# Performance work log

Measured on AMD Instinct MI355X. Metric: run time of the kernel, lower is better.

Reference implementation:

```python
import math
import jax, jax.numpy as jnp
import numpy as np

B, S, H, DQ, DV = 2, 2048, 16, 192, 128
NEG_INF = jnp.float32(-1e30)


def setup_inputs() -> dict:
    key = jax.random.key(0)
    kq, kk, kv = jax.random.split(key, 3)
    q = jax.random.normal(kq, (B, S, H, DQ), dtype=jnp.float32)
    k = jax.random.normal(kk, (B, S, H, DQ), dtype=jnp.float32)
    v = jax.random.normal(kv, (B, S, H, DV), dtype=jnp.float32)
    return {"q": q, "k": k, "v": v}


def reference(q, k, v):
    # Causal MLA attention, BSHD layout, asymmetric QK vs V head dims.
    dq = q.shape[-1]
    scale = jnp.asarray(math.sqrt(1.0 / dq), dtype=q.dtype)  # default 1/sqrt(dq)
    # scores: [B, H, S, S]
    scores = jnp.einsum("bqhd,bkhd->bhqk", q, k) * scale
    s = q.shape[1]
    causal = jnp.tril(jnp.ones((s, s), dtype=bool))  # qidx >= kidx
    scores = jnp.where(causal[None, None, :, :], scores, NEG_INF)
    p = jax.nn.softmax(scores, axis=-1)
    # out: [B, S, H, DV]
    out = jnp.einsum("bhqk,bkhd->bqhd", p, v)
    return out
```

## Files before the change

### kernel.cpp

```cpp
#include <hip/hip_runtime.h>

#define B_ 2
#define S_ 2048
#define H_ 16
#define DQ_ 192
#define DV_ 128
#define SCL2 0.10411163731422901f

typedef short short8 __attribute__((ext_vector_type(8)));
typedef float f32x4 __attribute__((ext_vector_type(4)));
typedef unsigned uint2v __attribute__((ext_vector_type(2)));

#define KG_BYTES ((size_t)25165824)
#define VG_BYTES ((size_t)16777216)

__device__ __forceinline__ unsigned short f2bf(float f) {
  union { float f; unsigned u; } x; x.f = f;
  unsigned r = x.u + 0x7FFFu + ((x.u >> 16) & 1u);
  return (unsigned short)(r >> 16);
}

__device__ __forceinline__ float hw_exp2(float x) {
  float r; asm("v_exp_f32 %0, %1" : "=v"(r) : "v"(x)); return r;
}
__device__ __forceinline__ unsigned cvtpk(float lo, float hi) {
  unsigned r; asm("v_cvt_pk_bf16_f32 %0, %1, %2" : "=v"(r) : "v"(lo), "v"(hi)); return r;
}
__device__ __forceinline__ float pl32max(float x) {
  uint2v r = __builtin_amdgcn_permlane32_swap(__float_as_uint(x), __float_as_uint(x), false, false);
  return fmaxf(__uint_as_float(r[0]), __uint_as_float(r[1]));
}
__device__ __forceinline__ float pl32add(float x) {
  uint2v r = __builtin_amdgcn_permlane32_swap(__float_as_uint(x), __float_as_uint(x), false, false);
  return __uint_as_float(r[0]) + __uint_as_float(r[1]);
}

#define GLL16(src, dst) \
  __builtin_amdgcn_global_load_lds((const __attribute__((address_space(1))) void*)(src), \
                                   (__attribute__((address_space(3))) void*)(dst), 16, 0, 0)

__global__ __launch_bounds__(256) void prep_k(const float* __restrict__ K,
                                              unsigned short* __restrict__ Kg) {
  int idx = blockIdx.x * 256 + threadIdx.x;
  int d4 = idx % 48; int r = idx / 48;
  int h = r % H_; r /= H_;
  int s = r % S_; int b = r / S_;
  float4 f = *(const float4*)(K + (size_t)((b * S_ + s) * H_ + h) * DQ_ + d4 * 4);
  ushort4 u; u.x = f2bf(f.x); u.y = f2bf(f.y); u.z = f2bf(f.z); u.w = f2bf(f.w);
  size_t rowb = (size_t)((b * H_ + h) * S_ + s) * (DQ_ * 2);
  int cb = (d4 * 8) ^ ((s & 7) << 4);
  *(ushort4*)((char*)Kg + rowb + cb) = u;
}

__global__ __launch_bounds__(256) void prep_v(const float* __restrict__ V,
                                              unsigned short* __restrict__ Vg) {
  __shared__ float lv[32][132];
  int blk = blockIdx.x;
  int sb = blk & 63, bh = blk >> 6;
  int b = bh >> 4, h = bh & 15;
  int tid = threadIdx.x;
  #pragma unroll
  for (int i = 0; i < 4; ++i) {
    int idx = i * 256 + tid;
    int s_in = idx >> 5, d4 = idx & 31;
    float4 f = *(const float4*)(V + (size_t)((b * S_ + sb * 32 + s_in) * H_ + h) * DV_ + d4 * 4);
    lv[s_in][d4 * 4 + 0] = f.x; lv[s_in][d4 * 4 + 1] = f.y;
    lv[s_in][d4 * 4 + 2] = f.z; lv[s_in][d4 * 4 + 3] = f.w;
  }
  __syncthreads();
  char* base = (char*)Vg + (size_t)blk * 8192;
  #pragma unroll
  for (int j = 0; j < 2; ++j) {
    int ob = tid * 32 + j * 16;
    int row = ob >> 7, cb = ob & 127;
    int orig = cb ^ ((row & 7) << 4);
    int d = row * 2 + (orig >> 6);
    int s0 = (orig & 63) >> 1;
    short8 u;
    #pragma unroll
    for (int e = 0; e < 8; ++e) u[e] = (short)f2bf(lv[s0 + e][d]);
    *(short8*)(base + ob) = u;
  }
}

__launch_bounds__(256, 2)
__global__ void mla_fwd(const float* __restrict__ Q,
                        const unsigned short* __restrict__ Kg,
                        const unsigned short* __restrict__ Vg,
                        float* __restrict__ O) {
  __shared__ __align__(16) unsigned char SB[2][20480];

  const int tid  = threadIdx.x;
  const int wid  = tid >> 6;
  const int lane = tid & 63;
  const int l15  = lane & 15;
  const int g    = lane >> 4;

  const int i  = blockIdx.x;
  const int x  = i & 7;
  const int li = i >> 3;
  const int j  = li & 15;
  const int bh = x * 4 + (li >> 4);
  const int b  = bh >> 4, h = bh & 15;

  const char* kg_bh = (const char*)Kg + (size_t)bh * S_ * (DQ_ * 2);
  const char* vg_bh = (const char*)Vg + (size_t)bh * 64 * 8192;

  const int kxor = (l15 & 7) << 4;
  const int g16  = g * 16;
  const int vlane = 12288 + (l15 >> 1) * 128 +
                    ((((l15 & 1) * 64) + g16) ^ (((l15 >> 1) & 7) << 4));
  const int sA = l15 + ((lane & 16) << 1);
  const int sB = sA + 16;
  const bool up = lane >= 32;

  #define STAGE(buf)                                         \
    do {                                                     \
      _Pragma("unroll")                                      \
      for (int ci = 0; ci < 5; ++ci) {                       \
        GLL16(sp[ci], &SB[buf][sdo[ci]]);                    \
        sp[ci] += sst[ci];                                   \
      }                                                      \
    } while (0)

  for (int job = 0; job < 2; ++job) {
    const int qtile = job ? j : (31 - j);
    const int q0w = qtile * 64 + wid * 16;

    short8 aq[6];
    {
      const size_t qoff = (size_t)((b * S_ + (q0w + l15)) * H_ + h) * DQ_;
      #pragma unroll
      for (int d0 = 0; d0 < 6; ++d0) {
        const float* p = Q + qoff + d0 * 32 + g * 8;
        float4 f0 = *(const float4*)(p);
        float4 f1 = *(const float4*)(p + 4);
        short8 a;
        a[0] = f2bf(f0.x * SCL2); a[1] = f2bf(f0.y * SCL2);
        a[2] = f2bf(f0.z * SCL2); a[3] = f2bf(f0.w * SCL2);
        a[4] = f2bf(f1.x * SCL2); a[5] = f2bf(f1.y * SCL2);
        a[6] = f2bf(f1.z * SCL2); a[7] = f2bf(f1.w * SCL2);
        aq[d0] = a;
      }
    }

    f32x4 o[8];
    #pragma unroll
    for (int t2 = 0; t2 < 8; ++t2) o[t2] = (f32x4)0.0f;
    float m = -1e30f, l = 0.0f;

    const int ntiles = qtile * 2 + 2;

    const char* sp[5];
    int sdo[5], sst[5];
    #pragma unroll
    for (int ci = 0; ci < 5; ++ci) {
      int cc = wid * 5 + ci;
      if (cc < 12) { sp[ci] = kg_bh + cc * 1024 + lane * 16;        sdo[ci] = cc * 1024;                sst[ci] = 12288; }
      else         { sp[ci] = vg_bh + (cc - 12) * 1024 + lane * 16; sdo[ci] = 12288 + (cc - 12) * 1024; sst[ci] = 8192; }
    }

    STAGE(0);
    __syncthreads();

    int cur = 0;
    for (int kt = 0; kt < ntiles; ++kt) {
      const int kbase = kt * 32;
      if (kt + 1 < ntiles) STAGE(cur ^ 1);

      const char* k0 = (const char*)&SB[cur][0] + l15 * 384;
      const char* k1 = k0 + 16 * 384;
      f32x4 sa0 = (f32x4)0.0f, sa1 = (f32x4)0.0f;
      __builtin_amdgcn_s_setprio(1);
      #pragma unroll
      for (int d0 = 0; d0 < 6; ++d0) {
        const int col = (d0 * 64 + g16) ^ kxor;
        short8 b0 = *(const short8*)(k0 + col);
        sa0 = __builtin_amdgcn_mfma_f32_16x16x32_bf16(b0, aq[d0], sa0, 0, 0, 0);
        short8 b1 = *(const short8*)(k1 + col);
        sa1 = __builtin_amdgcn_mfma_f32_16x16x32_bf16(b1, aq[d0], sa1, 0, 0, 0);
      }
      __builtin_amdgcn_s_setprio(0);

      const char* vbp = (const char*)&SB[cur][0] + vlane;
      short8 vb0 = *(const short8*)(vbp);
      short8 vb1 = *(const short8*)(vbp + 1024);
      short8 vb2 = *(const short8*)(vbp + 2048);
      short8 vb3 = *(const short8*)(vbp + 3072);

      float p[8];
      #pragma unroll
      for (int r = 0; r < 4; ++r) { p[r] = sa0[r]; p[4 + r] = sa1[r]; }
      if (kbase + 31 > q0w) {
        const int rem = q0w + l15 - kbase - 4 * g;
        #pragma unroll
        for (int r = 0; r < 4; ++r) {
          if (r > rem)      p[r]     = -1e30f;
          if (16 + r > rem) p[4 + r] = -1e30f;
        }
      }

      float mx = fmaxf(fmaxf(fmaxf(p[0], p[1]), fmaxf(p[2], p[3])),
                       fmaxf(fmaxf(p[4], p[5]), fmaxf(p[6], p[7])));
      mx = fmaxf(mx, __shfl_xor(mx, 16));
      mx = pl32max(mx);
      if (__any(mx > m + 8.0f)) {
        float mn = fmaxf(m, mx);
        float al = hw_exp2(m - mn);
        #pragma unroll
        for (int t2 = 0; t2 < 8; ++t2) o[t2] *= al;
        l *= al; m = mn;
      }
      #pragma unroll
      for (int jj = 0; jj < 8; ++jj) p[jj] = hw_exp2(p[jj] - m);
      l += ((p[0] + p[1]) + (p[2] + p[3])) + ((p[4] + p[5]) + (p[6] + p[7]));

      unsigned pk0 = cvtpk(p[0], p[1]);
      unsigned pk1 = cvtpk(p[2], p[3]);
      unsigned pk2 = cvtpk(p[4], p[5]);
      unsigned pk3 = cvtpk(p[6], p[7]);
      unsigned lo0 = __shfl(pk0, sA), hi0 = __shfl(pk2, sA);
      unsigned lo1 = __shfl(pk1, sA), hi1 = __shfl(pk3, sA);
      unsigned lo2 = __shfl(pk0, sB), hi2 = __shfl(pk2, sB);
      unsigned lo3 = __shfl(pk1, sB), hi3 = __shfl(pk3, sB);
      short8 vb4 = *(const short8*)(vbp + 4096);
      short8 vb5 = *(const short8*)(vbp + 5120);
      short8 vb6 = *(const short8*)(vbp + 6144);
      short8 vb7 = *(const short8*)(vbp + 7168);
      union { unsigned u[4]; short8 s; } pb;
      pb.u[0] = up ? hi0 : lo0;
      pb.u[1] = up ? hi1 : lo1;
      pb.u[2] = up ? hi2 : lo2;
      pb.u[3] = up ? hi3 : lo3;

      __builtin_amdgcn_s_setprio(1);
      o[0] = __builtin_amdgcn_mfma_f32_16x16x32_bf16(vb0, pb.s, o[0], 0, 0, 0);
      o[1] = __builtin_amdgcn_mfma_f32_16x16x32_bf16(vb1, pb.s, o[1], 0, 0, 0);
      o[2] = __builtin_amdgcn_mfma_f32_16x16x32_bf16(vb2, pb.s, o[2], 0, 0, 0);
      o[3] = __builtin_amdgcn_mfma_f32_16x16x32_bf16(vb3, pb.s, o[3], 0, 0, 0);
      o[4] = __builtin_amdgcn_mfma_f32_16x16x32_bf16(vb4, pb.s, o[4], 0, 0, 0);
      o[5] = __builtin_amdgcn_mfma_f32_16x16x32_bf16(vb5, pb.s, o[5], 0, 0, 0);
      o[6] = __builtin_amdgcn_mfma_f32_16x16x32_bf16(vb6, pb.s, o[6], 0, 0, 0);
      o[7] = __builtin_amdgcn_mfma_f32_16x16x32_bf16(vb7, pb.s, o[7], 0, 0, 0);
      __builtin_amdgcn_s_setprio(0);

      __syncthreads();
      cur ^= 1;
    }

    {
      float ll = l + __shfl_xor(l, 16);
      ll = pl32add(ll);
      const int q = q0w + l15;
      const float inv = 1.0f / ll;
      float* ob = O + (size_t)((b * S_ + q) * H_ + h) * DV_ + 4 * g;
      #pragma unroll
      for (int t2 = 0; t2 < 8; ++t2) {
        float4 st = { o[t2][0] * inv, o[t2][1] * inv, o[t2][2] * inv, o[t2][3] * inv };
        *(float4*)(ob + 16 * t2) = st;
      }
    }
  }
  #undef STAGE
}

__launch_bounds__(256)
__global__ void mla_fwd_fb(const float* __restrict__ Q,
                           const float* __restrict__ K,
                           const float* __restrict__ V,
                           float* __restrict__ O) {
  __shared__ __align__(16) unsigned short Kl[2][32][200];
  __shared__ __align__(16) unsigned short Vt[2][128][40];
  __shared__ __align__(16) unsigned short Pl[4][16][40];
  const int tid = threadIdx.x, wid = tid >> 6, lane = tid & 63;
  const int l15 = lane & 15, g = lane >> 4;
  const int qtile = (int)gridDim.x - 1 - (int)blockIdx.x;
  const int bh = blockIdx.y, b = bh >> 4, h = bh & 15;
  const int q0w = qtile * 64 + wid * 16;
  const int krs = H_ * DQ_, vrs = H_ * DV_;
  short8 aq[6];
  {
    const int qoff = ((b * S_ + (q0w + l15)) * H_ + h) * DQ_;
    #pragma unroll
    for (int d0 = 0; d0 < 6; ++d0) {
      const float* p = Q + qoff + d0 * 32 + g * 8;
      float4 f0 = *(const float4*)(p); float4 f1 = *(const float4*)(p + 4);
      short8 a;
      a[0]=f2bf(f0.x); a[1]=f2bf(f0.y); a[2]=f2bf(f0.z); a[3]=f2bf(f0.w);
      a[4]=f2bf(f1.x); a[5]=f2bf(f1.y); a[6]=f2bf(f1.z); a[7]=f2bf(f1.w);
      aq[d0] = a;
    }
  }
  f32x4 o[8];
  #pragma unroll
  for (int t = 0; t < 8; ++t) o[t] = (f32x4)0.0f;
  float m[4], l[4];
  #pragma unroll
  for (int r = 0; r < 4; ++r) { m[r] = -1e30f; l[r] = 0.0f; }
  const int ntiles = qtile * 2 + 2;
  float4 kr[6], vr[4];
  {
    const float* Kb = K + ((b * S_) * H_ + h) * DQ_;
    #pragma unroll
    for (int i = 0; i < 6; ++i) { int idx = i*256+tid; int row = idx/48, c4 = idx%48;
      kr[i] = *(const float4*)(Kb + row*krs + c4*4); }
    const float* Vb = V + ((b * S_) * H_ + h) * DV_;
    #pragma unroll
    for (int i = 0; i < 4; ++i) { int idx = i*256+tid; int row = idx&31, c4 = idx>>5;
      vr[i] = *(const float4*)(Vb + row*vrs + c4*4); }
    #pragma unroll
    for (int i = 0; i < 6; ++i) { int idx = i*256+tid; int row = idx/48, c4 = idx%48;
      ushort4 u; u.x=f2bf(kr[i].x); u.y=f2bf(kr[i].y); u.z=f2bf(kr[i].z); u.w=f2bf(kr[i].w);
      *(ushort4*)&Kl[0][row][c4*4] = u; }
    #pragma unroll
    for (int i = 0; i < 4; ++i) { int idx = i*256+tid; int row = idx&31, c4 = idx>>5;
      Vt[0][c4*4+0][row]=f2bf(vr[i].x); Vt[0][c4*4+1][row]=f2bf(vr[i].y);
      Vt[0][c4*4+2][row]=f2bf(vr[i].z); Vt[0][c4*4+3][row]=f2bf(vr[i].w); }
  }
  __syncthreads();
  int cur = 0;
  for (int kt = 0; kt < ntiles; ++kt) {
    const int kbase = kt * 32;
    const bool pf = (kt + 1 < ntiles);
    if (pf) {
      const int nb = kbase + 32;
      const float* Kb = K + ((b*S_+nb)*H_ + h)*DQ_;
      #pragma unroll
      for (int i = 0; i < 6; ++i) { int idx = i*256+tid; int row = idx/48, c4 = idx%48;
        kr[i] = *(const float4*)(Kb + row*krs + c4*4); }
      const float* Vb = V + ((b*S_+nb)*H_ + h)*DV_;
      #pragma unroll
      for (int i = 0; i < 4; ++i) { int idx = i*256+tid; int row = idx&31, c4 = idx>>5;
        vr[i] = *(const float4*)(Vb + row*vrs + c4*4); }
    }
    f32x4 sa0 = (f32x4)0.0f, sa1 = (f32x4)0.0f;
    #pragma unroll
    for (int d0 = 0; d0 < 6; ++d0) {
      short8 b0 = *(const short8*)&Kl[cur][l15][d0*32 + g*8];
      sa0 = __builtin_amdgcn_mfma_f32_16x16x32_bf16(aq[d0], b0, sa0, 0, 0, 0);
      short8 b1 = *(const short8*)&Kl[cur][16+l15][d0*32 + g*8];
      sa1 = __builtin_amdgcn_mfma_f32_16x16x32_bf16(aq[d0], b1, sa1, 0, 0, 0);
    }
    float p0[4], p1[4];
    #pragma unroll
    for (int r = 0; r < 4; ++r) {
      const int qg = q0w + 4*g + r;
      float s0 = sa0[r]*SCL2, s1 = sa1[r]*SCL2;
      if (kbase + l15 > qg) s0 = -1e30f;
      if (kbase + 16 + l15 > qg) s1 = -1e30f;
      p0[r] = s0; p1[r] = s1;
    }
    #pragma unroll
    for (int r = 0; r < 4; ++r) {
      float rm = fmaxf(p0[r], p1[r]);
      #pragma unroll
      for (int off = 1; off < 16; off <<= 1) rm = fmaxf(rm, __shfl_xor(rm, off));
      float mn = fmaxf(m[r], rm);
      float alpha = exp2f(m[r] - mn); m[r] = mn;
      float e0 = exp2f(p0[r] - mn), e1 = exp2f(p1[r] - mn);
      p0[r] = e0; p1[r] = e1;
      float rsum = e0 + e1;
      #pragma unroll
      for (int off = 1; off < 16; off <<= 1) rsum += __shfl_xor(rsum, off);
      l[r] = l[r]*alpha + rsum;
      #pragma unroll
      for (int t = 0; t < 8; ++t) o[t][r] *= alpha;
    }
    #pragma unroll
    for (int r = 0; r < 4; ++r) {
      Pl[wid][4*g+r][l15]      = f2bf(p0[r]);
      Pl[wid][4*g+r][16+l15]   = f2bf(p1[r]);
    }
    short8 pa = *(const short8*)&Pl[wid][l15][g*8];
    #pragma unroll
    for (int t = 0; t < 8; ++t) {
      short8 vb = *(const short8*)&Vt[cur][t*16+l15][g*8];
      o[t] = __builtin_amdgcn_mfma_f32_16x16x32_bf16(pa, vb, o[t], 0, 0, 0);
    }
    if (pf) {
      #pragma unroll
      for (int i = 0; i < 6; ++i) { int idx = i*256+tid; int row = idx/48, c4 = idx%48;
        ushort4 u; u.x=f2bf(kr[i].x); u.y=f2bf(kr[i].y); u.z=f2bf(kr[i].z); u.w=f2bf(kr[i].w);
        *(ushort4*)&Kl[cur^1][row][c4*4] = u; }
      #pragma unroll
      for (int i = 0; i < 4; ++i) { int idx = i*256+tid; int row = idx&31, c4 = idx>>5;
        Vt[cur^1][c4*4+0][row]=f2bf(vr[i].x); Vt[cur^1][c4*4+1][row]=f2bf(vr[i].y);
        Vt[cur^1][c4*4+2][row]=f2bf(vr[i].z); Vt[cur^1][c4*4+3][row]=f2bf(vr[i].w); }
    }
    __syncthreads();
    cur ^= 1;
  }
  #pragma unroll
  for (int r = 0; r < 4; ++r) {
    const int qg = q0w + 4*g + r;
    const float inv = 1.0f / l[r];
    #pragma unroll
    for (int t = 0; t < 8; ++t)
      O[((b*S_+qg)*H_ + h)*DV_ + t*16 + l15] = o[t][r] * inv;
  }
}

extern "C" void kernel_launch(void* const* d_in, const int* in_sizes, int n_in,
                              void* d_out, int out_size, void* d_ws, size_t ws_size,
                              hipStream_t stream) {
  const float* q = (const float*)d_in[0];
  const float* k = (const float*)d_in[1];
  const float* v = (const float*)d_in[2];
  float* out = (float*)d_out;

  if (ws_size >= KG_BYTES + VG_BYTES) {
    unsigned short* Kg = (unsigned short*)d_ws;
    unsigned short* Vg = (unsigned short*)((char*)d_ws + KG_BYTES);
    prep_k<<<dim3((B_ * S_ * H_ * 48) / 256), dim3(256), 0, stream>>>(k, Kg);
    prep_v<<<dim3(B_ * H_ * 64), dim3(256), 0, stream>>>(v, Vg);
    mla_fwd<<<dim3(512), dim3(256), 0, stream>>>(q, Kg, Vg, out);
  } else {
    dim3 grid(S_ / 64, B_ * H_);
    mla_fwd_fb<<<grid, dim3(256), 0, stream>>>(q, k, v, out);
  }
}
```

Before: 106.2 us.

## Switch attention to 32x32 MFMA with 128-row query tiles and 64-key stages

```diff
diff --git a/kernel.cpp b/kernel.cpp
--- a/kernel.cpp
+++ b/kernel.cpp
@@ -9,6 +9,7 @@
 
 typedef short short8 __attribute__((ext_vector_type(8)));
 typedef float f32x4 __attribute__((ext_vector_type(4)));
+typedef float f32x16 __attribute__((ext_vector_type(16)));
 typedef unsigned uint2v __attribute__((ext_vector_type(2)));
 
 #define KG_BYTES ((size_t)25165824)
@@ -54,32 +55,32 @@
 
 __global__ __launch_bounds__(256) void prep_v(const float* __restrict__ V,
                                               unsigned short* __restrict__ Vg) {
-  __shared__ float lv[32][132];
+  __shared__ float lv[64][132];
   int blk = blockIdx.x;
-  int sb = blk & 63, bh = blk >> 6;
+  int tile = blk & 31, bh = blk >> 5;
   int b = bh >> 4, h = bh & 15;
   int tid = threadIdx.x;
   #pragma unroll
-  for (int i = 0; i < 4; ++i) {
-    int idx = i * 256 + tid;
+  for (int it = 0; it < 8; ++it) {
+    int idx = it * 256 + tid;
     int s_in = idx >> 5, d4 = idx & 31;
-    float4 f = *(const float4*)(V + (size_t)((b * S_ + sb * 32 + s_in) * H_ + h) * DV_ + d4 * 4);
+    float4 f = *(const float4*)(V + (size_t)((b * S_ + tile * 64 + s_in) * H_ + h) * DV_ + d4 * 4);
     lv[s_in][d4 * 4 + 0] = f.x; lv[s_in][d4 * 4 + 1] = f.y;
     lv[s_in][d4 * 4 + 2] = f.z; lv[s_in][d4 * 4 + 3] = f.w;
   }
   __syncthreads();
-  char* base = (char*)Vg + (size_t)blk * 8192;
-  #pragma unroll
-  for (int j = 0; j < 2; ++j) {
-    int ob = tid * 32 + j * 16;
-    int row = ob >> 7, cb = ob & 127;
-    int orig = cb ^ ((row & 7) << 4);
-    int d = row * 2 + (orig >> 6);
-    int s0 = (orig & 63) >> 1;
+  char* base = (char*)Vg + (size_t)blk * 16384;
+  #pragma unroll
+  for (int it = 0; it < 4; ++it) {
+    int ch = it * 256 + tid;
+    int pr = ch >> 4, ci = ch & 15;
+    int orig = ci ^ (pr & 15);
+    int dv = pr * 2 + (orig >> 3);
+    int k0 = (orig & 7) * 8;
     short8 u;
     #pragma unroll
-    for (int e = 0; e < 8; ++e) u[e] = (short)f2bf(lv[s0 + e][d]);
-    *(short8*)(base + ob) = u;
+    for (int e = 0; e < 8; ++e) u[e] = (short)f2bf(lv[k0 + e][dv]);
+    *(short8*)(base + ch * 16) = u;
   }
 }
 
@@ -88,180 +89,177 @@
                         const unsigned short* __restrict__ Kg,
                         const unsigned short* __restrict__ Vg,
                         float* __restrict__ O) {
-  __shared__ __align__(16) unsigned char SB[2][20480];
+  __shared__ __align__(16) unsigned char SB[2][40960];
 
   const int tid  = threadIdx.x;
   const int wid  = tid >> 6;
   const int lane = tid & 63;
-  const int l15  = lane & 15;
-  const int g    = lane >> 4;
+  const int l31  = lane & 31;
+  const int hi   = lane >> 5;
+  const int hi16 = hi * 16;
 
   const int i  = blockIdx.x;
   const int x  = i & 7;
   const int li = i >> 3;
-  const int j  = li & 15;
-  const int bh = x * 4 + (li >> 4);
+  const int r_ = li >> 5;
+  const int c  = li & 31;
+  const int bh = x * 4 + (c >> 3);
+  const int jj = c & 7;
+  const int qtile = r_ ? jj : (15 - jj);
   const int b  = bh >> 4, h = bh & 15;
 
   const char* kg_bh = (const char*)Kg + (size_t)bh * S_ * (DQ_ * 2);
-  const char* vg_bh = (const char*)Vg + (size_t)bh * 64 * 8192;
-
-  const int kxor = (l15 & 7) << 4;
-  const int g16  = g * 16;
-  const int vlane = 12288 + (l15 >> 1) * 128 +
-                    ((((l15 & 1) * 64) + g16) ^ (((l15 >> 1) & 7) << 4));
-  const int sA = l15 + ((lane & 16) << 1);
-  const int sB = sA + 16;
-  const bool up = lane >= 32;
-
-  #define STAGE(buf)                                         \
-    do {                                                     \
-      _Pragma("unroll")                                      \
-      for (int ci = 0; ci < 5; ++ci) {                       \
-        GLL16(sp[ci], &SB[buf][sdo[ci]]);                    \
-        sp[ci] += sst[ci];                                   \
-      }                                                      \
+  const char* vg_bh = (const char*)Vg + (size_t)bh * 32 * 16384;
+
+  const int wq0 = qtile * 128 + wid * 32;
+  const int qln = wq0 + l31;
+
+  short8 qf[12];
+  {
+    const size_t qoff = (size_t)((b * S_ + qln) * H_ + h) * DQ_;
+    #pragma unroll
+    for (int d0 = 0; d0 < 12; ++d0) {
+      const float* p = Q + qoff + d0 * 16 + hi * 8;
+      float4 f0 = *(const float4*)(p);
+      float4 f1 = *(const float4*)(p + 4);
+      short8 a;
+      a[0] = f2bf(f0.x * SCL2); a[1] = f2bf(f0.y * SCL2);
+      a[2] = f2bf(f0.z * SCL2); a[3] = f2bf(f0.w * SCL2);
+      a[4] = f2bf(f1.x * SCL2); a[5] = f2bf(f1.y * SCL2);
+      a[6] = f2bf(f1.z * SCL2); a[7] = f2bf(f1.w * SCL2);
+      qf[d0] = a;
+    }
+  }
+
+  f32x16 o[4];
+  #pragma unroll
+  for (int t2 = 0; t2 < 4; ++t2) o[t2] = (f32x16)0.0f;
+  float m = -1e30f, l = 0.0f;
+
+  const int kxor = (lane & 7) << 4;
+  const int prl  = l31 >> 1;
+  const int nb_  = (lane & 1) * 8 + hi;
+  int voff[2][2];
+  #pragma unroll
+  for (int kh = 0; kh < 2; ++kh)
+    #pragma unroll
+    for (int ks = 0; ks < 2; ++ks) {
+      int n = nb_ + kh * 4 + ks * 2;
+      voff[kh][ks] = prl * 256 + ((n ^ prl) << 4);
+    }
+
+  const int ntiles = 2 * qtile + 2;
+
+  const char* kS = kg_bh + wid * 10240 + lane * 16;
+  const char* vS = vg_bh - 24576 + wid * 10240 + lane * 16;
+
+  #define STAGE(buf)                                                       \
+    do {                                                                   \
+      _Pragma("unroll")                                                    \
+      for (int ci = 0; ci < 10; ++ci) {                                    \
+        const int cc = wid * 10 + ci;                                      \
+        const char* src = (cc < 24) ? (kS + ci * 1024) : (vS + ci * 1024); \
+        GLL16(src, &SB[buf][cc * 1024]);                                   \
+      }                                                                    \
     } while (0)
 
-  for (int job = 0; job < 2; ++job) {
-    const int qtile = job ? j : (31 - j);
-    const int q0w = qtile * 64 + wid * 16;
-
-    short8 aq[6];
-    {
-      const size_t qoff = (size_t)((b * S_ + (q0w + l15)) * H_ + h) * DQ_;
-      #pragma unroll
-      for (int d0 = 0; d0 < 6; ++d0) {
-        const float* p = Q + qoff + d0 * 32 + g * 8;
-        float4 f0 = *(const float4*)(p);
-        float4 f1 = *(const float4*)(p + 4);
-        short8 a;
-        a[0] = f2bf(f0.x * SCL2); a[1] = f2bf(f0.y * SCL2);
-        a[2] = f2bf(f0.z * SCL2); a[3] = f2bf(f0.w * SCL2);
-        a[4] = f2bf(f1.x * SCL2); a[5] = f2bf(f1.y * SCL2);
-        a[6] = f2bf(f1.z * SCL2); a[7] = f2bf(f1.w * SCL2);
-        aq[d0] = a;
-      }
-    }
-
-    f32x4 o[8];
-    #pragma unroll
-    for (int t2 = 0; t2 < 8; ++t2) o[t2] = (f32x4)0.0f;
-    float m = -1e30f, l = 0.0f;
-
-    const int ntiles = qtile * 2 + 2;
-
-    const char* sp[5];
-    int sdo[5], sst[5];
-    #pragma unroll
-    for (int ci = 0; ci < 5; ++ci) {
-      int cc = wid * 5 + ci;
-      if (cc < 12) { sp[ci] = kg_bh + cc * 1024 + lane * 16;        sdo[ci] = cc * 1024;                sst[ci] = 12288; }
-      else         { sp[ci] = vg_bh + (cc - 12) * 1024 + lane * 16; sdo[ci] = 12288 + (cc - 12) * 1024; sst[ci] = 8192; }
-    }
-
-    STAGE(0);
-    __syncthreads();
-
-    int cur = 0;
-    for (int kt = 0; kt < ntiles; ++kt) {
-      const int kbase = kt * 32;
-      if (kt + 1 < ntiles) STAGE(cur ^ 1);
-
-      const char* k0 = (const char*)&SB[cur][0] + l15 * 384;
-      const char* k1 = k0 + 16 * 384;
-      f32x4 sa0 = (f32x4)0.0f, sa1 = (f32x4)0.0f;
+  #define HALF(S, KH)                                                             \
+    {                                                                             \
+      const int khb = kbase + (KH) * 32;                                          \
+      if (khb <= wq0 + 31) {                                                      \
+        float p_[16];                                                             \
+        _Pragma("unroll") for (int r = 0; r < 16; ++r) p_[r] = S[r];              \
+        if (khb + 31 > wq0) {                                                     \
+          const int rem = qln - khb - 4 * hi;                                     \
+          _Pragma("unroll") for (int r = 0; r < 16; ++r) {                        \
+            const int kof = (r & 3) + 8 * (r >> 2);                               \
+            if (kof > rem) p_[r] = -1e30f;                                        \
+          }                                                                       \
+        }                                                                         \
+        float mx = p_[0];                                                         \
+        _Pragma("unroll") for (int r = 1; r < 16; ++r) mx = fmaxf(mx, p_[r]);     \
+        mx = pl32max(mx);                                                         \
+        if (__any(mx > m + 8.0f)) {                                               \
+          float mn = fmaxf(m, mx);                                                \
+          float al = hw_exp2(m - mn);                                             \
+          _Pragma("unroll") for (int t2 = 0; t2 < 4; ++t2) o[t2] *= al;           \
+          l *= al; m = mn;                                                        \
+        }                                                                         \
+        _Pragma("unroll") for (int r = 0; r < 16; ++r) p_[r] = hw_exp2(p_[r] - m);\
+        float sum_ = 0.0f;                                                        \
+        _Pragma("unroll") for (int r = 0; r < 16; ++r) sum_ += p_[r];             \
+        l += sum_;                                                                \
+        unsigned a_ = cvtpk(p_[0], p_[1]),   b2_ = cvtpk(p_[2], p_[3]);           \
+        unsigned c_ = cvtpk(p_[4], p_[5]),   d_  = cvtpk(p_[6], p_[7]);           \
+        unsigned e_ = cvtpk(p_[8], p_[9]),   f_  = cvtpk(p_[10], p_[11]);         \
+        unsigned g_ = cvtpk(p_[12], p_[13]), h_  = cvtpk(p_[14], p_[15]);         \
+        uint2v s02 = __builtin_amdgcn_permlane32_swap(a_, c_, false, false);      \
+        uint2v s13 = __builtin_amdgcn_permlane32_swap(b2_, d_, false, false);     \
+        uint2v s46 = __builtin_amdgcn_permlane32_swap(e_, g_, false, false);      \
+        uint2v s57 = __builtin_amdgcn_permlane32_swap(f_, h_, false, false);      \
+        union { unsigned u[4]; short8 s; } pb0, pb1;                              \
+        pb0.u[0] = s02[0]; pb0.u[1] = s13[0]; pb0.u[2] = s02[1]; pb0.u[3] = s13[1];\
+        pb1.u[0] = s46[0]; pb1.u[1] = s57[0]; pb1.u[2] = s46[1]; pb1.u[3] = s57[1];\
+        __builtin_amdgcn_s_setprio(1);                                            \
+        _Pragma("unroll") for (int t2 = 0; t2 < 4; ++t2) {                        \
+          short8 va0 = *(const short8*)(vbb + t2 * 4096 + voff[KH][0]);           \
+          o[t2] = __builtin_amdgcn_mfma_f32_32x32x16_bf16(va0, pb0.s, o[t2], 0, 0, 0); \
+          short8 va1 = *(const short8*)(vbb + t2 * 4096 + voff[KH][1]);           \
+          o[t2] = __builtin_amdgcn_mfma_f32_32x32x16_bf16(va1, pb1.s, o[t2], 0, 0, 0); \
+        }                                                                         \
+        __builtin_amdgcn_s_setprio(0);                                            \
+      }                                                                           \
+    }
+
+  STAGE(0); kS += 24576; vS += 16384;
+  __syncthreads();
+
+  int cur = 0;
+  for (int kt = 0; kt < ntiles; ++kt) {
+    const int kbase = kt * 64;
+    if (kt + 1 < ntiles) { STAGE(cur ^ 1); kS += 24576; vS += 16384; }
+
+    const unsigned char* kb  = SB[cur];
+    const unsigned char* vbb = SB[cur] + 24576;
+    const bool active = (kbase <= wq0 + 31);
+
+    if (active) {
+      const char* kr0 = (const char*)kb + l31 * 384;
+      const char* kr1 = kr0 + 32 * 384;
+      f32x16 s0 = (f32x16)0.0f, s1 = (f32x16)0.0f;
       __builtin_amdgcn_s_setprio(1);
       #pragma unroll
-      for (int d0 = 0; d0 < 6; ++d0) {
-        const int col = (d0 * 64 + g16) ^ kxor;
-        short8 b0 = *(const short8*)(k0 + col);
-        sa0 = __builtin_amdgcn_mfma_f32_16x16x32_bf16(b0, aq[d0], sa0, 0, 0, 0);
-        short8 b1 = *(const short8*)(k1 + col);
-        sa1 = __builtin_amdgcn_mfma_f32_16x16x32_bf16(b1, aq[d0], sa1, 0, 0, 0);
+      for (int d0 = 0; d0 < 12; ++d0) {
+        const int col = (d0 * 32 + hi16) ^ kxor;
+        s0 = __builtin_amdgcn_mfma_f32_32x32x16_bf16(*(const short8*)(kr0 + col), qf[d0], s0, 0, 0, 0);
+        s1 = __builtin_amdgcn_mfma_f32_32x32x16_bf16(*(const short8*)(kr1 + col), qf[d0], s1, 0, 0, 0);
       }
       __builtin_amdgcn_s_setprio(0);
 
-      const char* vbp = (const char*)&SB[cur][0] + vlane;
-      short8 vb0 = *(const short8*)(vbp);
-      short8 vb1 = *(const short8*)(vbp + 1024);
-      short8 vb2 = *(const short8*)(vbp + 2048);
-      short8 vb3 = *(const short8*)(vbp + 3072);
-
-      float p[8];
-      #pragma unroll
-      for (int r = 0; r < 4; ++r) { p[r] = sa0[r]; p[4 + r] = sa1[r]; }
-      if (kbase + 31 > q0w) {
-        const int rem = q0w + l15 - kbase - 4 * g;
-        #pragma unroll
-        for (int r = 0; r < 4; ++r) {
-          if (r > rem)      p[r]     = -1e30f;
-          if (16 + r > rem) p[4 + r] = -1e30f;
-        }
+      HALF(s0, 0)
+      HALF(s1, 1)
+    }
+
+    __syncthreads();
+    cur ^= 1;
+  }
+
+  {
+    float ll = pl32add(l);
+    const float inv = 1.0f / ll;
+    float* ob = O + (size_t)((b * S_ + qln) * H_ + h) * DV_;
+    #pragma unroll
+    for (int t2 = 0; t2 < 4; ++t2) {
+      #pragma unroll
+      for (int rr = 0; rr < 4; ++rr) {
+        float4 st = { o[t2][rr * 4 + 0] * inv, o[t2][rr * 4 + 1] * inv,
+                      o[t2][rr * 4 + 2] * inv, o[t2][rr * 4 + 3] * inv };
+        *(float4*)(ob + t2 * 32 + rr * 8 + hi * 4) = st;
       }
-
-      float mx = fmaxf(fmaxf(fmaxf(p[0], p[1]), fmaxf(p[2], p[3])),
-                       fmaxf(fmaxf(p[4], p[5]), fmaxf(p[6], p[7])));
-      mx = fmaxf(mx, __shfl_xor(mx, 16));
-      mx = pl32max(mx);
-      if (__any(mx > m + 8.0f)) {
-        float mn = fmaxf(m, mx);
-        float al = hw_exp2(m - mn);
-        #pragma unroll
-        for (int t2 = 0; t2 < 8; ++t2) o[t2] *= al;
-        l *= al; m = mn;
-      }
-      #pragma unroll
-      for (int jj = 0; jj < 8; ++jj) p[jj] = hw_exp2(p[jj] - m);
-      l += ((p[0] + p[1]) + (p[2] + p[3])) + ((p[4] + p[5]) + (p[6] + p[7]));
-
-      unsigned pk0 = cvtpk(p[0], p[1]);
-      unsigned pk1 = cvtpk(p[2], p[3]);
-      unsigned pk2 = cvtpk(p[4], p[5]);
-      unsigned pk3 = cvtpk(p[6], p[7]);
-      unsigned lo0 = __shfl(pk0, sA), hi0 = __shfl(pk2, sA);
-      unsigned lo1 = __shfl(pk1, sA), hi1 = __shfl(pk3, sA);
-      unsigned lo2 = __shfl(pk0, sB), hi2 = __shfl(pk2, sB);
-      unsigned lo3 = __shfl(pk1, sB), hi3 = __shfl(pk3, sB);
-      short8 vb4 = *(const short8*)(vbp + 4096);
-      short8 vb5 = *(const short8*)(vbp + 5120);
-      short8 vb6 = *(const short8*)(vbp + 6144);
-      short8 vb7 = *(const short8*)(vbp + 7168);
-      union { unsigned u[4]; short8 s; } pb;
-      pb.u[0] = up ? hi0 : lo0;
-      pb.u[1] = up ? hi1 : lo1;
-      pb.u[2] = up ? hi2 : lo2;
-      pb.u[3] = up ? hi3 : lo3;
-
-      __builtin_amdgcn_s_setprio(1);
-      o[0] = __builtin_amdgcn_mfma_f32_16x16x32_bf16(vb0, pb.s, o[0], 0, 0, 0);
-      o[1] = __builtin_amdgcn_mfma_f32_16x16x32_bf16(vb1, pb.s, o[1], 0, 0, 0);
-      o[2] = __builtin_amdgcn_mfma_f32_16x16x32_bf16(vb2, pb.s, o[2], 0, 0, 0);
-      o[3] = __builtin_amdgcn_mfma_f32_16x16x32_bf16(vb3, pb.s, o[3], 0, 0, 0);
-      o[4] = __builtin_amdgcn_mfma_f32_16x16x32_bf16(vb4, pb.s, o[4], 0, 0, 0);
-      o[5] = __builtin_amdgcn_mfma_f32_16x16x32_bf16(vb5, pb.s, o[5], 0, 0, 0);
-      o[6] = __builtin_amdgcn_mfma_f32_16x16x32_bf16(vb6, pb.s, o[6], 0, 0, 0);
-      o[7] = __builtin_amdgcn_mfma_f32_16x16x32_bf16(vb7, pb.s, o[7], 0, 0, 0);
-      __builtin_amdgcn_s_setprio(0);
-
-      __syncthreads();
-      cur ^= 1;
-    }
-
-    {
-      float ll = l + __shfl_xor(l, 16);
-      ll = pl32add(ll);
-      const int q = q0w + l15;
-      const float inv = 1.0f / ll;
-      float* ob = O + (size_t)((b * S_ + q) * H_ + h) * DV_ + 4 * g;
-      #pragma unroll
-      for (int t2 = 0; t2 < 8; ++t2) {
-        float4 st = { o[t2][0] * inv, o[t2][1] * inv, o[t2][2] * inv, o[t2][3] * inv };
-        *(float4*)(ob + 16 * t2) = st;
-      }
     }
   }
   #undef STAGE
+  #undef HALF
 }
 
 __launch_bounds__(256)
@@ -412,7 +410,7 @@
     unsigned short* Kg = (unsigned short*)d_ws;
     unsigned short* Vg = (unsigned short*)((char*)d_ws + KG_BYTES);
     prep_k<<<dim3((B_ * S_ * H_ * 48) / 256), dim3(256), 0, stream>>>(k, Kg);
-    prep_v<<<dim3(B_ * H_ * 64), dim3(256), 0, stream>>>(v, Vg);
+    prep_v<<<dim3(B_ * H_ * 32), dim3(256), 0, stream>>>(v, Vg);
     mla_fwd<<<dim3(512), dim3(256), 0, stream>>>(q, Kg, Vg, out);
   } else {
     dim3 grid(S_ / 64, B_ * H_);
```

New measurement: 94.97 us. 1.12x faster.
